# Kernel tuning notes

Measured on AMD Instinct MI355X. Metric: run time of the kernel, lower is better.

Reference implementation:

```python
import jax, jax.numpy as jnp
import numpy as np

D_MODEL = 1024
NUM_HEADS = 16
D_K = D_MODEL // NUM_HEADS


def setup_inputs() -> dict:
    key = jax.random.key(0)
    ks = jax.random.split(key, 11)
    B, S = 2, 2048
    scale = 1.0 / np.sqrt(D_MODEL)
    inp = {
        'Q': jax.random.normal(ks[0], (B, S, D_MODEL), dtype=jnp.float32),
        'K': jax.random.normal(ks[1], (B, S, D_MODEL), dtype=jnp.float32),
        'V': jax.random.normal(ks[2], (B, S, D_MODEL), dtype=jnp.float32),
        'Wq': jax.random.normal(ks[3], (D_MODEL, D_MODEL), dtype=jnp.float32) * scale,
        'bq': jax.random.normal(ks[4], (D_MODEL,), dtype=jnp.float32) * scale,
        'Wk': jax.random.normal(ks[5], (D_MODEL, D_MODEL), dtype=jnp.float32) * scale,
        'bk': jax.random.normal(ks[6], (D_MODEL,), dtype=jnp.float32) * scale,
        'Wv': jax.random.normal(ks[7], (D_MODEL, D_MODEL), dtype=jnp.float32) * scale,
        'bv': jax.random.normal(ks[8], (D_MODEL,), dtype=jnp.float32) * scale,
        'Wo': jax.random.normal(ks[9], (D_MODEL, D_MODEL), dtype=jnp.float32) * scale,
        'bo': jax.random.normal(ks[10], (D_MODEL,), dtype=jnp.float32) * scale,
    }
    return inp


def _split_heads(x):
    B, S, _ = x.shape
    return x.reshape(B, S, NUM_HEADS, D_K).transpose(0, 2, 1, 3)  # [B,H,S,dk]


def reference(Q, K, V, Wq, bq, Wk, bk, Wv, bv, Wo, bo):
    # Linear projections (torch Linear: x @ W.T + b)
    q = _split_heads(Q @ Wq.T + bq)
    k = _split_heads(K @ Wk.T + bk)
    v = _split_heads(V @ Wv.T + bv)
    scores = jnp.einsum('bhqd,bhkd->bhqk', q, k) / jnp.sqrt(jnp.float32(D_K))
    probs = jax.nn.softmax(scores, axis=-1)
    out = jnp.einsum('bhqk,bhkd->bhqd', probs, v)  # [B,H,S,dk]
    B, H, S, dk = out.shape
    out = out.transpose(0, 2, 1, 3).reshape(B, S, D_MODEL)
    return out @ Wo.T + bo
```

## Files before the change

### kernel.cpp

```cpp
#include <hip/hip_runtime.h>
#include <hip/hip_bf16.h>

#define DEV __device__ __forceinline__

#define BATCH 2
#define SEQ   2048
#define DMODEL 1024
#define NHEAD 16
#define DK    64
#define MROWS (BATCH*SEQ)
#define KD    1024
#define GEMM_NT (KD/32)

#define QSCALE 0.18033688011112042f

typedef __attribute__((ext_vector_type(4))) float f32x4;
typedef __attribute__((ext_vector_type(8))) short s16x8;
typedef __attribute__((ext_vector_type(4))) float fvec4;
typedef __attribute__((ext_vector_type(2))) unsigned int u32x2;
typedef __attribute__((ext_vector_type(4))) unsigned int u32x4;

__device__ short g_X[3][MROWS*DMODEL];
__device__ short g_W[4][DMODEL*DMODEL];
__device__ short g_q [MROWS*DMODEL];
__device__ short g_k [MROWS*DMODEL];
__device__ short g_vt[MROWS*DMODEL];
__device__ short g_at[MROWS*DMODEL];

DEV short f2bf(float f) {
  union { __hip_bfloat16 h; short s; } u;
  u.h = __float2bfloat16(f);
  return u.s;
}

DEV unsigned int f2bf2(float lo, float hi) {
  unsigned int r;
  asm("v_cvt_pk_bf16_f32 %0, %1, %2" : "=v"(r) : "v"(lo), "v"(hi));
  return r;
}

DEV float fexp2(float x) {
  float r;
  asm("v_exp_f32 %0, %1" : "=v"(r) : "v"(x));
  return r;
}

DEV void gload_lds16(const void* g, void* l) {
  __builtin_amdgcn_global_load_lds(
      (const __attribute__((address_space(1))) void*)g,
      (__attribute__((address_space(3))) void*)l, 16, 0, 0);
}

DEV f32x4 mfma16(s16x8 a, s16x8 b, f32x4 c) {
  return __builtin_amdgcn_mfma_f32_16x16x32_bf16(a, b, c, 0, 0, 0);
}

__global__ __launch_bounds__(256)
void cast_all(const float* __restrict__ q, const float* __restrict__ k,
              const float* __restrict__ v, const float* __restrict__ wq,
              const float* __restrict__ wk, const float* __restrict__ wv,
              const float* __restrict__ wo) {
  int z = blockIdx.z;
  const float* src;
  short* dst;
  int n8;
  if (z < 3) {
    src = z == 0 ? q : z == 1 ? k : v;
    dst = g_X[z];
    n8 = MROWS*DMODEL/8;
  } else {
    src = z == 3 ? wq : z == 4 ? wk : z == 5 ? wv : wo;
    dst = g_W[z - 3];
    n8 = DMODEL*DMODEL/8;
  }
  int i = blockIdx.x * 256 + threadIdx.x;
  if (i < n8) {
    const fvec4* p = (const fvec4*)(src + (size_t)i*8);
    fvec4 v0 = p[0], v1 = p[1];
    u32x4 r;
    r[0] = f2bf2(v0[0], v0[1]); r[1] = f2bf2(v0[2], v0[3]);
    r[2] = f2bf2(v1[0], v1[1]); r[3] = f2bf2(v1[2], v1[3]);
    *(u32x4*)(dst + (size_t)i*8) = r;
  }
}

struct GemmSmem { short As[2][128*32]; short Bs[2][128*32]; };

DEV void gemm_core(GemmSmem& sm, const short* __restrict__ A,
                   const short* __restrict__ Bw, const float* __restrict__ bias,
                   void* __restrict__ outp, float scale, int mode,
                   int rowBase, int colBase) {
  const int t = threadIdx.x, l = t & 63, w = t >> 6, g = l >> 4;
  const int wr = w >> 1, wc = w & 1;

  f32x4 acc[4][4] = {};

  auto stage = [&](int buf, int k0) {
#pragma unroll
    for (int j = 0; j < 2; ++j) {
      int e = w*1024 + j*512 + l*8;
      int e2 = e ^ (((e >> 7) & 3) << 3);
      int r = e2 >> 5, c = e2 & 31;
      gload_lds16(A  + (size_t)(rowBase + r)*KD + k0 + c, &sm.As[buf][w*1024 + j*512]);
      gload_lds16(Bw + (size_t)(colBase + r)*KD + k0 + c, &sm.Bs[buf][w*1024 + j*512]);
    }
  };

  stage(0, 0);
  stage(1, 32);

  for (int i = 0; i < GEMM_NT; ++i) {
    if (i < GEMM_NT - 1) asm volatile("s_waitcnt vmcnt(4)" ::: "memory");
    else                 asm volatile("s_waitcnt vmcnt(0)" ::: "memory");
    __builtin_amdgcn_s_barrier();
    __builtin_amdgcn_sched_barrier(0);

    const int cur = i & 1;
    s16x8 a[4], b[4];
#pragma unroll
    for (int x = 0; x < 4; ++x) {
      int ra = wr*64 + x*16 + (l & 15);
      int ia = (ra*32 + g*8) ^ (((ra >> 2) & 3) << 3);
      a[x] = *(const s16x8*)&sm.As[cur][ia];
      int rb = wc*64 + x*16 + (l & 15);
      int ib = (rb*32 + g*8) ^ (((rb >> 2) & 3) << 3);
      b[x] = *(const s16x8*)&sm.Bs[cur][ib];
    }

    __builtin_amdgcn_s_setprio(1);
#pragma unroll
    for (int x = 0; x < 4; ++x)
#pragma unroll
      for (int jn = 0; jn < 4; ++jn)
        acc[x][jn] = mfma16(a[x], b[jn], acc[x][jn]);
    __builtin_amdgcn_s_setprio(0);

    __builtin_amdgcn_s_barrier();
    __builtin_amdgcn_sched_barrier(0);
    if (i + 2 < GEMM_NT) stage(cur, (i + 2)*32);
  }

#pragma unroll
  for (int x = 0; x < 4; ++x) {
    int mrow0 = rowBase + wr*64 + x*16 + g*4;
#pragma unroll
    for (int jn = 0; jn < 4; ++jn) {
      int n = colBase + wc*64 + jn*16 + (l & 15);
      float bv = bias[n];
      float val[4];
#pragma unroll
      for (int r = 0; r < 4; ++r) val[r] = (acc[x][jn][r] + bv) * scale;
      if (mode == 3) {
#pragma unroll
        for (int r = 0; r < 4; ++r)
          ((float*)outp)[(size_t)(mrow0 + r)*DMODEL + n] = val[r];
      } else {
        unsigned int pk0 = f2bf2(val[0], val[1]);
        unsigned int pk1 = f2bf2(val[2], val[3]);
        int h = n >> 6, d = n & 63;
#pragma unroll
        for (int r = 0; r < 4; ++r) {
          int m = mrow0 + r;
          int b = m >> 11, s = m & 2047;
          unsigned int pk = r < 2 ? pk0 : pk1;
          short sv = (short)((r & 1) ? (pk >> 16) : (pk & 0xffff));
          if (mode == 1)
            ((short*)outp)[(((size_t)(b*NHEAD + h)*SEQ + s)*DK) + d] = sv;
          else
            ((short*)outp)[((size_t)(b*NHEAD + h)*DK + d)*SEQ + s] = sv;
        }
      }
    }
  }
}

__global__ __launch_bounds__(256, 4)
void proj_qkv(const float* __restrict__ bq, const float* __restrict__ bk,
              const float* __restrict__ bv) {
  __shared__ GemmSmem sm;
  int z = blockIdx.z;
  int orig = blockIdx.y*8 + blockIdx.x;
  int swz = (orig & 7)*32 + (orig >> 3);
  int bx = swz & 7, by = swz >> 3;
  const float* bias = z == 0 ? bq : z == 1 ? bk : bv;
  void* outp = z == 0 ? (void*)g_q : z == 1 ? (void*)g_k : (void*)g_vt;
  gemm_core(sm, g_X[z], g_W[z], bias, outp, z == 0 ? QSCALE : 1.0f,
            z == 2 ? 2 : 1, by*128, bx*128);
}

__global__ __launch_bounds__(256, 4)
void proj_out(const float* __restrict__ bo, float* __restrict__ out) {
  __shared__ GemmSmem sm;
  int orig = blockIdx.y*8 + blockIdx.x;
  int swz = (orig & 7)*32 + (orig >> 3);
  int bx = swz & 7, by = swz >> 3;
  gemm_core(sm, g_at, g_W[3], bo, out, 1.0f, 3, by*128, bx*128);
}

__global__ __launch_bounds__(512, 4)
void attn_kernel(short* __restrict__ aout) {
  __shared__ short ks[4][64*64];
  __shared__ short vs[4][64*64];

  const int t = threadIdx.x, l = t & 63, w = t >> 6, g = l >> 4;
  const int q15 = l & 15;
  const int qg = w & 3, kp = w >> 2;
  int orig = blockIdx.y*16 + blockIdx.x;
  int swz = (orig & 7)*64 + (orig >> 3);
  const int qblk = swz & 15, bh = swz >> 4;
  const int qbase = qblk * 128;
  const size_t hoff = (size_t)bh * SEQ * DK;

  auto stage_pair = [&](int pr) {
    int e = t*8;
    int e2 = e ^ (((e >> 6) & 7) << 3);
    int t0 = 2*pr, t1 = t0 + 1;
    gload_lds16(g_k + hoff + (size_t)(t0*64)*DK + e2, &ks[t0 & 3][e]);
    gload_lds16(g_k + hoff + (size_t)(t1*64)*DK + e2, &ks[t1 & 3][e]);
    gload_lds16(g_vt + hoff + (size_t)(e2 >> 6)*SEQ + t0*64 + (e2 & 63), &vs[t0 & 3][e]);
    gload_lds16(g_vt + hoff + (size_t)(e2 >> 6)*SEQ + t1*64 + (e2 & 63), &vs[t1 & 3][e]);
  };

  s16x8 qf[2][2];
  {
    const short* q0 = g_q + hoff + (size_t)(qbase + qg*32 + q15)*DK;
    qf[0][0] = *(const s16x8*)(q0 + g*8);
    qf[0][1] = *(const s16x8*)(q0 + 32 + g*8);
    qf[1][0] = *(const s16x8*)(q0 + 16*DK + g*8);
    qf[1][1] = *(const s16x8*)(q0 + 16*DK + 32 + g*8);
  }
  stage_pair(0);

  float lsum[2] = {0.f, 0.f};
  f32x4 o[2][4] = {};

  for (int i = 0; i < 16; ++i) {
    asm volatile("s_waitcnt vmcnt(0)" ::: "memory");
    __builtin_amdgcn_s_barrier();
    __builtin_amdgcn_sched_barrier(0);
    if (i + 1 < 16) stage_pair(i + 1);

    const short* kb = ks[(2*i + kp) & 3];
    const short* vb = vs[(2*i + kp) & 3];

    f32x4 sc[2][4] = {};
    __builtin_amdgcn_s_setprio(1);
#pragma unroll
    for (int ni = 0; ni < 4; ++ni) {
      int row = ni*16 + q15;
      int sx = (row & 7) << 3;
      s16x8 k0 = *(const s16x8*)&kb[(row*64 + g*8) ^ sx];
      s16x8 k1 = *(const s16x8*)&kb[(row*64 + 32 + g*8) ^ sx];
      sc[0][ni] = mfma16(k0, qf[0][0], sc[0][ni]);
      sc[0][ni] = mfma16(k1, qf[0][1], sc[0][ni]);
      sc[1][ni] = mfma16(k0, qf[1][0], sc[1][ni]);
      sc[1][ni] = mfma16(k1, qf[1][1], sc[1][ni]);
    }
    __builtin_amdgcn_s_setprio(0);

    s16x8 pa[2][2];
#pragma unroll
    for (int grp = 0; grp < 2; ++grp) {
      float p[4][4];
#pragma unroll
      for (int ni = 0; ni < 4; ++ni)
#pragma unroll
        for (int r = 0; r < 4; ++r)
          p[ni][r] = fexp2(sc[grp][ni][r]);
      float s0 = (p[0][0]+p[0][1]) + (p[0][2]+p[0][3]);
      float s1 = (p[1][0]+p[1][1]) + (p[1][2]+p[1][3]);
      float s2 = (p[2][0]+p[2][1]) + (p[2][2]+p[2][3]);
      float s3 = (p[3][0]+p[3][1]) + (p[3][2]+p[3][3]);
      lsum[grp] += (s0+s1) + (s2+s3);

      unsigned pk[4][2];
#pragma unroll
      for (int ni = 0; ni < 4; ++ni) {
        pk[ni][0] = f2bf2(p[ni][0], p[ni][1]);
        pk[ni][1] = f2bf2(p[ni][2], p[ni][3]);
      }
#pragma unroll
      for (int kf = 0; kf < 2; ++kf) {
        u32x4 P4;
#pragma unroll
        for (int u = 0; u < 2; ++u) {
          unsigned x = pk[2*kf][u], y = pk[2*kf + 1][u];
          asm("v_permlane32_swap_b32 %0, %1" : "+v"(x), "+v"(y));
          asm("v_permlane16_swap_b32 %0, %1" : "+v"(x), "+v"(y));
          P4[u]     = x;
          P4[2 + u] = y;
        }
        union { u32x4 u4; s16x8 s8; } cv;
        cv.u4 = P4;
        pa[grp][kf] = cv.s8;
      }
    }

    __builtin_amdgcn_s_setprio(1);
#pragma unroll
    for (int nd = 0; nd < 4; ++nd) {
      int row = nd*16 + q15;
      int sx = (row & 7) << 3;
      s16x8 v0 = *(const s16x8*)&vb[(row*64 + g*8) ^ sx];
      s16x8 v1 = *(const s16x8*)&vb[(row*64 + 32 + g*8) ^ sx];
      o[0][nd] = mfma16(pa[0][0], v0, o[0][nd]);
      o[0][nd] = mfma16(pa[0][1], v1, o[0][nd]);
      o[1][nd] = mfma16(pa[1][0], v0, o[1][nd]);
      o[1][nd] = mfma16(pa[1][1], v1, o[1][nd]);
    }
    __builtin_amdgcn_s_setprio(0);
  }

  __syncthreads();
  float* ob = (float*)&vs[0][0];
  float* lb = (float*)&ks[0][0];
  if (kp) {
#pragma unroll
    for (int grp = 0; grp < 2; ++grp) {
#pragma unroll
      for (int nd = 0; nd < 4; ++nd)
#pragma unroll
        for (int r = 0; r < 4; ++r)
          ob[(qg*32 + grp*16 + nd*4 + r)*64 + l] = o[grp][nd][r];
      lb[(qg*2 + grp)*64 + l] = lsum[grp];
    }
  }
  __syncthreads();
  if (!kp) {
    int b = bh >> 4, h = bh & 15;
#pragma unroll
    for (int grp = 0; grp < 2; ++grp) {
#pragma unroll
      for (int nd = 0; nd < 4; ++nd)
#pragma unroll
        for (int r = 0; r < 4; ++r)
          o[grp][nd][r] += ob[(qg*32 + grp*16 + nd*4 + r)*64 + l];
      float ls = lsum[grp] + lb[(qg*2 + grp)*64 + l];
      ls += __shfl_xor(ls, 16);
      ls += __shfl_xor(ls, 32);
      float inv = 1.0f / ls;
      float iv[4];
#pragma unroll
      for (int r = 0; r < 4; ++r)
        iv[r] = __shfl(inv, (l & 48) | (g*4 + r));
#pragma unroll
      for (int nd = 0; nd < 4; ++nd) {
        int dcol = h*DK + nd*16 + q15;
#pragma unroll
        for (int r = 0; r < 4; ++r) {
          int srow = qbase + qg*32 + grp*16 + g*4 + r;
          aout[((size_t)(b*SEQ + srow))*DMODEL + dcol] = f2bf(o[grp][nd][r] * iv[r]);
        }
      }
    }
  }
}

extern "C" void kernel_launch(void* const* d_in, const int* in_sizes, int n_in,
                              void* d_out, int out_size, void* d_ws, size_t ws_size,
                              hipStream_t stream) {
  const float* Q  = (const float*)d_in[0];
  const float* K  = (const float*)d_in[1];
  const float* V  = (const float*)d_in[2];
  const float* Wq = (const float*)d_in[3];
  const float* bq = (const float*)d_in[4];
  const float* Wk = (const float*)d_in[5];
  const float* bk = (const float*)d_in[6];
  const float* Wv = (const float*)d_in[7];
  const float* bv = (const float*)d_in[8];
  const float* Wo = (const float*)d_in[9];
  const float* bo = (const float*)d_in[10];

  short* pat;
  hipGetSymbolAddress((void**)&pat, HIP_SYMBOL(g_at));

  const int nX8 = MROWS*DMODEL/8;
  dim3 blk(256);

  cast_all<<<dim3(nX8/256, 1, 7), blk, 0, stream>>>(Q, K, V, Wq, Wk, Wv, Wo);
  proj_qkv<<<dim3(DMODEL/128, MROWS/128, 3), blk, 0, stream>>>(bq, bk, bv);
  attn_kernel<<<dim3(SEQ/128, BATCH*NHEAD), dim3(512), 0, stream>>>(pat);
  proj_out<<<dim3(DMODEL/128, MROWS/128), blk, 0, stream>>>(bo, (float*)d_out);
}
```

Baseline: 136.4 us.

## Use 256x256 tiles with triple-buffered LDS pipeline for QKV projection GEMM

Replaces the shared 128x128 GEMM core for the QKV projections with a dedicated 512-thread kernel that computes 256x256 output tiles, using a 3-stage LDS buffer and split half-tile loads interleaved with MFMA phases. The larger tile raises arithmetic intensity and cuts global reloads, and the deeper pipeline aims to hide load latency. The grid shrinks to 192 blocks, which may underfill the 256 CUs and raises register and LDS pressure. The output projection is specialised inline with its epilogue simplified to fp32 stores.

```diff
diff --git a/kernel.cpp b/kernel.cpp
--- a/kernel.cpp
+++ b/kernel.cpp
@@ -84,14 +84,138 @@
   }
 }
 
+struct Gemm8Smem { short As[3][256*32]; short Bs[3][256*32]; };
+
+__global__ __launch_bounds__(512, 2)
+void proj_qkv(const float* __restrict__ bq, const float* __restrict__ bk,
+              const float* __restrict__ bv) {
+  __shared__ Gemm8Smem sm;
+  const int t = threadIdx.x, l = t & 63, g = l >> 4, q15 = l & 15;
+  const int w = t >> 6, wm = w >> 2, wn = w & 3;
+  const int z = blockIdx.z;
+  const short* A  = g_X[z];
+  const short* Bw = g_W[z];
+  const float* bias = z == 0 ? bq : z == 1 ? bk : bv;
+  void* outp = z == 0 ? (void*)g_q : z == 1 ? (void*)g_k : (void*)g_vt;
+  const float scale = z == 0 ? QSCALE : 1.0f;
+  const int mode = z == 2 ? 2 : 1;
+  const int rowBase = blockIdx.y * 256;
+  const int colBase = blockIdx.x * 256;
+
+  f32x4 acc[8][4] = {};
+
+  auto stageA = [&](int buf, int tt, int m) {
+    int e = m*4096 + t*8;
+    int e2 = e ^ (((e >> 7) & 3) << 3);
+    gload_lds16(A + (size_t)(rowBase + (e2 >> 5))*KD + tt*32 + (e2 & 31),
+                &sm.As[buf][e]);
+  };
+  auto stageB = [&](int buf, int tt, int m) {
+    int e = m*4096 + t*8;
+    int e2 = e ^ (((e >> 7) & 3) << 3);
+    gload_lds16(Bw + (size_t)(colBase + (e2 >> 5))*KD + tt*32 + (e2 & 31),
+                &sm.Bs[buf][e]);
+  };
+
+  stageA(0, 0, 0); stageB(0, 0, 0); stageA(0, 0, 1); stageB(0, 0, 1);
+  stageA(1, 1, 0); stageB(1, 1, 0); stageA(1, 1, 1); stageB(1, 1, 1);
+  asm volatile("s_waitcnt vmcnt(4)" ::: "memory");
+  __builtin_amdgcn_s_barrier();
+  __builtin_amdgcn_sched_barrier(0);
+
+  int cur = 0, nxt = 2;
+  for (int i = 0; i < GEMM_NT; ++i) {
+    const int tt2 = (i + 2) & (GEMM_NT - 1);
+
+    s16x8 a[8], b[2];
+#pragma unroll
+    for (int mf = 0; mf < 8; ++mf) {
+      int row = wm*128 + mf*16 + q15;
+      a[mf] = *(const s16x8*)&sm.As[cur][(row*32 + g*8) ^ (((row >> 2) & 3) << 3)];
+    }
+#pragma unroll
+    for (int nf = 0; nf < 2; ++nf) {
+      int row = wn*64 + nf*16 + q15;
+      b[nf] = *(const s16x8*)&sm.Bs[cur][(row*32 + g*8) ^ (((row >> 2) & 3) << 3)];
+    }
+    stageA(nxt, tt2, 0); stageB(nxt, tt2, 0);
+    __builtin_amdgcn_s_barrier();
+    __builtin_amdgcn_sched_barrier(0);
+    __builtin_amdgcn_s_setprio(1);
+#pragma unroll
+    for (int mf = 0; mf < 8; ++mf)
+#pragma unroll
+      for (int nf = 0; nf < 2; ++nf)
+        acc[mf][nf] = mfma16(a[mf], b[nf], acc[mf][nf]);
+    __builtin_amdgcn_s_setprio(0);
+    __builtin_amdgcn_s_barrier();
+    __builtin_amdgcn_sched_barrier(0);
+
+#pragma unroll
+    for (int nf = 0; nf < 2; ++nf) {
+      int row = wn*64 + (nf + 2)*16 + q15;
+      b[nf] = *(const s16x8*)&sm.Bs[cur][(row*32 + g*8) ^ (((row >> 2) & 3) << 3)];
+    }
+    stageA(nxt, tt2, 1); stageB(nxt, tt2, 1);
+    __builtin_amdgcn_s_barrier();
+    __builtin_amdgcn_sched_barrier(0);
+    __builtin_amdgcn_s_setprio(1);
+#pragma unroll
+    for (int mf = 0; mf < 8; ++mf)
+#pragma unroll
+      for (int nf = 0; nf < 2; ++nf)
+        acc[mf][nf + 2] = mfma16(a[mf], b[nf], acc[mf][nf + 2]);
+    __builtin_amdgcn_s_setprio(0);
+    asm volatile("s_waitcnt vmcnt(4)" ::: "memory");
+    __builtin_amdgcn_s_barrier();
+    __builtin_amdgcn_sched_barrier(0);
+
+    cur = cur == 2 ? 0 : cur + 1;
+    nxt = nxt == 2 ? 0 : nxt + 1;
+  }
+  asm volatile("s_waitcnt vmcnt(0)" ::: "memory");
+
+#pragma unroll
+  for (int mf = 0; mf < 8; ++mf) {
+    int mrow0 = rowBase + wm*128 + mf*16 + g*4;
+#pragma unroll
+    for (int nf = 0; nf < 4; ++nf) {
+      int n = colBase + wn*64 + nf*16 + q15;
+      float bv = bias[n];
+      float val[4];
+#pragma unroll
+      for (int r = 0; r < 4; ++r) val[r] = (acc[mf][nf][r] + bv) * scale;
+      unsigned int pk0 = f2bf2(val[0], val[1]);
+      unsigned int pk1 = f2bf2(val[2], val[3]);
+      int h = n >> 6, d = n & 63;
+#pragma unroll
+      for (int r = 0; r < 4; ++r) {
+        int m = mrow0 + r;
+        int b = m >> 11, s = m & 2047;
+        unsigned int pk = r < 2 ? pk0 : pk1;
+        short sv = (short)((r & 1) ? (pk >> 16) : (pk & 0xffff));
+        if (mode == 1)
+          ((short*)outp)[(((size_t)(b*NHEAD + h)*SEQ + s)*DK) + d] = sv;
+        else
+          ((short*)outp)[((size_t)(b*NHEAD + h)*DK + d)*SEQ + s] = sv;
+      }
+    }
+  }
+}
+
 struct GemmSmem { short As[2][128*32]; short Bs[2][128*32]; };
 
-DEV void gemm_core(GemmSmem& sm, const short* __restrict__ A,
-                   const short* __restrict__ Bw, const float* __restrict__ bias,
-                   void* __restrict__ outp, float scale, int mode,
-                   int rowBase, int colBase) {
+__global__ __launch_bounds__(256, 4)
+void proj_out(const float* __restrict__ bo, float* __restrict__ out) {
+  __shared__ GemmSmem sm;
   const int t = threadIdx.x, l = t & 63, w = t >> 6, g = l >> 4;
   const int wr = w >> 1, wc = w & 1;
+  int orig = blockIdx.y*8 + blockIdx.x;
+  int swz = (orig & 7)*32 + (orig >> 3);
+  int bx = swz & 7, by = swz >> 3;
+  const int rowBase = by*128, colBase = bx*128;
+  const short* A = g_at;
+  const short* Bw = g_W[3];
 
   f32x4 acc[4][4] = {};
 
@@ -146,55 +270,12 @@
 #pragma unroll
     for (int jn = 0; jn < 4; ++jn) {
       int n = colBase + wc*64 + jn*16 + (l & 15);
-      float bv = bias[n];
-      float val[4];
-#pragma unroll
-      for (int r = 0; r < 4; ++r) val[r] = (acc[x][jn][r] + bv) * scale;
-      if (mode == 3) {
-#pragma unroll
-        for (int r = 0; r < 4; ++r)
-          ((float*)outp)[(size_t)(mrow0 + r)*DMODEL + n] = val[r];
-      } else {
-        unsigned int pk0 = f2bf2(val[0], val[1]);
-        unsigned int pk1 = f2bf2(val[2], val[3]);
-        int h = n >> 6, d = n & 63;
-#pragma unroll
-        for (int r = 0; r < 4; ++r) {
-          int m = mrow0 + r;
-          int b = m >> 11, s = m & 2047;
-          unsigned int pk = r < 2 ? pk0 : pk1;
-          short sv = (short)((r & 1) ? (pk >> 16) : (pk & 0xffff));
-          if (mode == 1)
-            ((short*)outp)[(((size_t)(b*NHEAD + h)*SEQ + s)*DK) + d] = sv;
-          else
-            ((short*)outp)[((size_t)(b*NHEAD + h)*DK + d)*SEQ + s] = sv;
-        }
-      }
-    }
-  }
-}
-
-__global__ __launch_bounds__(256, 4)
-void proj_qkv(const float* __restrict__ bq, const float* __restrict__ bk,
-              const float* __restrict__ bv) {
-  __shared__ GemmSmem sm;
-  int z = blockIdx.z;
-  int orig = blockIdx.y*8 + blockIdx.x;
-  int swz = (orig & 7)*32 + (orig >> 3);
-  int bx = swz & 7, by = swz >> 3;
-  const float* bias = z == 0 ? bq : z == 1 ? bk : bv;
-  void* outp = z == 0 ? (void*)g_q : z == 1 ? (void*)g_k : (void*)g_vt;
-  gemm_core(sm, g_X[z], g_W[z], bias, outp, z == 0 ? QSCALE : 1.0f,
-            z == 2 ? 2 : 1, by*128, bx*128);
-}
-
-__global__ __launch_bounds__(256, 4)
-void proj_out(const float* __restrict__ bo, float* __restrict__ out) {
-  __shared__ GemmSmem sm;
-  int orig = blockIdx.y*8 + blockIdx.x;
-  int swz = (orig & 7)*32 + (orig >> 3);
-  int bx = swz & 7, by = swz >> 3;
-  gemm_core(sm, g_at, g_W[3], bo, out, 1.0f, 3, by*128, bx*128);
+      float bv = bo[n];
+#pragma unroll
+      for (int r = 0; r < 4; ++r)
+        out[(size_t)(mrow0 + r)*DMODEL + n] = acc[x][jn][r] + bv;
+    }
+  }
 }
 
 __global__ __launch_bounds__(512, 4)
@@ -378,7 +459,7 @@
   dim3 blk(256);
 
   cast_all<<<dim3(nX8/256, 1, 7), blk, 0, stream>>>(Q, K, V, Wq, Wk, Wv, Wo);
-  proj_qkv<<<dim3(DMODEL/128, MROWS/128, 3), blk, 0, stream>>>(bq, bk, bv);
+  proj_qkv<<<dim3(4, 16, 3), dim3(512), 0, stream>>>(bq, bk, bv);
   attn_kernel<<<dim3(SEQ/128, BATCH*NHEAD), dim3(512), 0, stream>>>(pat);
-  proj_out<<<dim3(DMODEL/128, MROWS/128), blk, 0, stream>>>(bo, (float*)d_out);
-}
+  proj_out<<<dim3(8, 32), blk, 0, stream>>>(bo, (float*)d_out);
+}
```

Measured after the change: 147.4 us. 1.08x slower.

## Triple-buffer GEMM LDS staging and split QKV projection into separate launches

Applied to the files above, without the earlier changes.

The projection GEMM moves from double to triple LDS buffering. The prefetch of tile i+2 is now issued right after the current tile's fragments are read, which removes the second barrier per K-step. The single 3D-grid QKV projection launch becomes three separate 256-block launches of one unified proj_gemm kernel, with pointers taken from symbol addresses on the host. In exchange, shared memory per block grows and launch bounds drop to 3 blocks per CU, and the three serial launches lose the concurrency of the 768-block grid.

```diff
diff --git a/kernel.cpp b/kernel.cpp
--- a/kernel.cpp
+++ b/kernel.cpp
@@ -84,14 +84,18 @@
   }
 }
 
-struct GemmSmem { short As[2][128*32]; short Bs[2][128*32]; };
-
-DEV void gemm_core(GemmSmem& sm, const short* __restrict__ A,
-                   const short* __restrict__ Bw, const float* __restrict__ bias,
-                   void* __restrict__ outp, float scale, int mode,
-                   int rowBase, int colBase) {
+struct GemmSmem { short As[3][128*32]; short Bs[3][128*32]; };
+
+__global__ __launch_bounds__(256, 3)
+void proj_gemm(const short* __restrict__ A, const short* __restrict__ Bw,
+               const float* __restrict__ bias, void* __restrict__ outp,
+               float scale, int mode) {
+  __shared__ GemmSmem sm;
   const int t = threadIdx.x, l = t & 63, w = t >> 6, g = l >> 4;
   const int wr = w >> 1, wc = w & 1;
+  int orig = blockIdx.y*8 + blockIdx.x;
+  int swz = (orig & 7)*32 + (orig >> 3);
+  const int rowBase = (swz >> 3)*128, colBase = (swz & 7)*128;
 
   f32x4 acc[4][4] = {};
 
@@ -109,13 +113,13 @@
   stage(0, 0);
   stage(1, 32);
 
+  int cur = 0, nxt = 2;
   for (int i = 0; i < GEMM_NT; ++i) {
     if (i < GEMM_NT - 1) asm volatile("s_waitcnt vmcnt(4)" ::: "memory");
     else                 asm volatile("s_waitcnt vmcnt(0)" ::: "memory");
     __builtin_amdgcn_s_barrier();
     __builtin_amdgcn_sched_barrier(0);
 
-    const int cur = i & 1;
     s16x8 a[4], b[4];
 #pragma unroll
     for (int x = 0; x < 4; ++x) {
@@ -126,6 +130,8 @@
       int ib = (rb*32 + g*8) ^ (((rb >> 2) & 3) << 3);
       b[x] = *(const s16x8*)&sm.Bs[cur][ib];
     }
+    if (i + 2 < GEMM_NT) stage(nxt, (i + 2)*32);
+    __builtin_amdgcn_sched_barrier(0);
 
     __builtin_amdgcn_s_setprio(1);
 #pragma unroll
@@ -135,9 +141,8 @@
         acc[x][jn] = mfma16(a[x], b[jn], acc[x][jn]);
     __builtin_amdgcn_s_setprio(0);
 
-    __builtin_amdgcn_s_barrier();
-    __builtin_amdgcn_sched_barrier(0);
-    if (i + 2 < GEMM_NT) stage(cur, (i + 2)*32);
+    cur = cur == 2 ? 0 : cur + 1;
+    nxt = nxt == 2 ? 0 : nxt + 1;
   }
 
 #pragma unroll
@@ -172,29 +177,6 @@
       }
     }
   }
-}
-
-__global__ __launch_bounds__(256, 4)
-void proj_qkv(const float* __restrict__ bq, const float* __restrict__ bk,
-              const float* __restrict__ bv) {
-  __shared__ GemmSmem sm;
-  int z = blockIdx.z;
-  int orig = blockIdx.y*8 + blockIdx.x;
-  int swz = (orig & 7)*32 + (orig >> 3);
-  int bx = swz & 7, by = swz >> 3;
-  const float* bias = z == 0 ? bq : z == 1 ? bk : bv;
-  void* outp = z == 0 ? (void*)g_q : z == 1 ? (void*)g_k : (void*)g_vt;
-  gemm_core(sm, g_X[z], g_W[z], bias, outp, z == 0 ? QSCALE : 1.0f,
-            z == 2 ? 2 : 1, by*128, bx*128);
-}
-
-__global__ __launch_bounds__(256, 4)
-void proj_out(const float* __restrict__ bo, float* __restrict__ out) {
-  __shared__ GemmSmem sm;
-  int orig = blockIdx.y*8 + blockIdx.x;
-  int swz = (orig & 7)*32 + (orig >> 3);
-  int bx = swz & 7, by = swz >> 3;
-  gemm_core(sm, g_at, g_W[3], bo, out, 1.0f, 3, by*128, bx*128);
 }
 
 __global__ __launch_bounds__(512, 4)
@@ -371,14 +353,24 @@
   const float* Wo = (const float*)d_in[9];
   const float* bo = (const float*)d_in[10];
 
-  short* pat;
+  short *pX, *pW, *pq, *pk, *pvt, *pat;
+  hipGetSymbolAddress((void**)&pX,  HIP_SYMBOL(g_X));
+  hipGetSymbolAddress((void**)&pW,  HIP_SYMBOL(g_W));
+  hipGetSymbolAddress((void**)&pq,  HIP_SYMBOL(g_q));
+  hipGetSymbolAddress((void**)&pk,  HIP_SYMBOL(g_k));
+  hipGetSymbolAddress((void**)&pvt, HIP_SYMBOL(g_vt));
   hipGetSymbolAddress((void**)&pat, HIP_SYMBOL(g_at));
 
   const int nX8 = MROWS*DMODEL/8;
+  const size_t NX = (size_t)MROWS*DMODEL;
+  const size_t NW = (size_t)DMODEL*DMODEL;
   dim3 blk(256);
+  dim3 gP(8, 32);
 
   cast_all<<<dim3(nX8/256, 1, 7), blk, 0, stream>>>(Q, K, V, Wq, Wk, Wv, Wo);
-  proj_qkv<<<dim3(DMODEL/128, MROWS/128, 3), blk, 0, stream>>>(bq, bk, bv);
+  proj_gemm<<<gP, blk, 0, stream>>>(pX,        pW,        bq, pq,  QSCALE, 1);
+  proj_gemm<<<gP, blk, 0, stream>>>(pX + NX,   pW + NW,   bk, pk,  1.0f,   1);
+  proj_gemm<<<gP, blk, 0, stream>>>(pX + 2*NX, pW + 2*NW, bv, pvt, 1.0f,   2);
   attn_kernel<<<dim3(SEQ/128, BATCH*NHEAD), dim3(512), 0, stream>>>(pat);
-  proj_out<<<dim3(DMODEL/128, MROWS/128), blk, 0, stream>>>(bo, (float*)d_out);
-}
+  proj_gemm<<<gP, blk, 0, stream>>>(pat, pW + 3*NW, bo, (float*)d_out, 1.0f, 3);
+}
```

Result: slower. 143.2 us (+5.0%).

## Triple-buffer GEMM LDS pipeline and stage V-transpose epilogue through LDS

Applied to the files above, without the earlier changes.

Moves the GEMM mainloop from double to triple buffering in LDS. The next-next tile is now issued right after the fragment reads, which removes the second barrier per k-step. The transposed V projection epilogue now writes bf16 results into LDS with an XOR swizzle and then stores 16-byte contiguous rows along the sequence, replacing scattered 2-byte global stores. The larger LDS footprint lowers launch bounds occupancy from 4 to 3 blocks per CU.

```diff
diff --git a/kernel.cpp b/kernel.cpp
--- a/kernel.cpp
+++ b/kernel.cpp
@@ -84,13 +84,14 @@
   }
 }
 
-struct GemmSmem { short As[2][128*32]; short Bs[2][128*32]; };
+struct GemmSmem { short As[3][128*32]; short Bs[3][128*32]; };
 
 DEV void gemm_core(GemmSmem& sm, const short* __restrict__ A,
                    const short* __restrict__ Bw, const float* __restrict__ bias,
                    void* __restrict__ outp, float scale, int mode,
                    int rowBase, int colBase) {
   const int t = threadIdx.x, l = t & 63, w = t >> 6, g = l >> 4;
+  const int q15 = l & 15;
   const int wr = w >> 1, wc = w & 1;
 
   f32x4 acc[4][4] = {};
@@ -109,23 +110,25 @@
   stage(0, 0);
   stage(1, 32);
 
+  int cur = 0, nxt = 2;
   for (int i = 0; i < GEMM_NT; ++i) {
     if (i < GEMM_NT - 1) asm volatile("s_waitcnt vmcnt(4)" ::: "memory");
     else                 asm volatile("s_waitcnt vmcnt(0)" ::: "memory");
     __builtin_amdgcn_s_barrier();
     __builtin_amdgcn_sched_barrier(0);
 
-    const int cur = i & 1;
     s16x8 a[4], b[4];
 #pragma unroll
     for (int x = 0; x < 4; ++x) {
-      int ra = wr*64 + x*16 + (l & 15);
+      int ra = wr*64 + x*16 + q15;
       int ia = (ra*32 + g*8) ^ (((ra >> 2) & 3) << 3);
       a[x] = *(const s16x8*)&sm.As[cur][ia];
-      int rb = wc*64 + x*16 + (l & 15);
+      int rb = wc*64 + x*16 + q15;
       int ib = (rb*32 + g*8) ^ (((rb >> 2) & 3) << 3);
       b[x] = *(const s16x8*)&sm.Bs[cur][ib];
     }
+    if (i + 2 < GEMM_NT) stage(nxt, (i + 2)*32);
+    __builtin_amdgcn_sched_barrier(0);
 
     __builtin_amdgcn_s_setprio(1);
 #pragma unroll
@@ -135,9 +138,40 @@
         acc[x][jn] = mfma16(a[x], b[jn], acc[x][jn]);
     __builtin_amdgcn_s_setprio(0);
 
-    __builtin_amdgcn_s_barrier();
-    __builtin_amdgcn_sched_barrier(0);
-    if (i + 2 < GEMM_NT) stage(cur, (i + 2)*32);
+    cur = cur == 2 ? 0 : cur + 1;
+    nxt = nxt == 2 ? 0 : nxt + 1;
+  }
+
+  if (mode == 2) {
+    short* ct = (short*)&sm;
+    __syncthreads();
+#pragma unroll
+    for (int x = 0; x < 4; ++x) {
+      int m0 = wr*64 + x*16 + g*4;
+#pragma unroll
+      for (int jn = 0; jn < 4; ++jn) {
+        int n = wc*64 + jn*16 + q15;
+        float bv = bias[colBase + n];
+        u32x2 w2;
+        w2[0] = f2bf2(acc[x][jn][0] + bv, acc[x][jn][1] + bv);
+        w2[1] = f2bf2(acc[x][jn][2] + bv, acc[x][jn][3] + bv);
+        int mi = m0 ^ ((n & 15) << 3);
+        *(u32x2*)&ct[n*128 + mi] = w2;
+      }
+    }
+    __syncthreads();
+    int c = t & 1, n = t >> 1;
+    int ng = colBase + n;
+    int h = ng >> 6, d = ng & 63;
+    int b = rowBase >> 11;
+    int s0 = (rowBase & 2047) + c*64;
+    short* dst = (short*)outp + ((size_t)(b*NHEAD + h)*DK + d)*SEQ + s0;
+#pragma unroll
+    for (int j = 0; j < 8; ++j) {
+      int mi = (c*64 + j*8) ^ ((n & 15) << 3);
+      *(s16x8*)&dst[j*8] = *(const s16x8*)&ct[n*128 + mi];
+    }
+    return;
   }
 
 #pragma unroll
@@ -145,7 +179,7 @@
     int mrow0 = rowBase + wr*64 + x*16 + g*4;
 #pragma unroll
     for (int jn = 0; jn < 4; ++jn) {
-      int n = colBase + wc*64 + jn*16 + (l & 15);
+      int n = colBase + wc*64 + jn*16 + q15;
       float bv = bias[n];
       float val[4];
 #pragma unroll
@@ -164,17 +198,14 @@
           int b = m >> 11, s = m & 2047;
           unsigned int pk = r < 2 ? pk0 : pk1;
           short sv = (short)((r & 1) ? (pk >> 16) : (pk & 0xffff));
-          if (mode == 1)
-            ((short*)outp)[(((size_t)(b*NHEAD + h)*SEQ + s)*DK) + d] = sv;
-          else
-            ((short*)outp)[((size_t)(b*NHEAD + h)*DK + d)*SEQ + s] = sv;
+          ((short*)outp)[(((size_t)(b*NHEAD + h)*SEQ + s)*DK) + d] = sv;
         }
       }
     }
   }
 }
 
-__global__ __launch_bounds__(256, 4)
+__global__ __launch_bounds__(256, 3)
 void proj_qkv(const float* __restrict__ bq, const float* __restrict__ bk,
               const float* __restrict__ bv) {
   __shared__ GemmSmem sm;
@@ -188,7 +219,7 @@
             z == 2 ? 2 : 1, by*128, bx*128);
 }
 
-__global__ __launch_bounds__(256, 4)
+__global__ __launch_bounds__(256, 3)
 void proj_out(const float* __restrict__ bo, float* __restrict__ out) {
   __shared__ GemmSmem sm;
   int orig = blockIdx.y*8 + blockIdx.x;
@@ -378,7 +409,7 @@
   dim3 blk(256);
 
   cast_all<<<dim3(nX8/256, 1, 7), blk, 0, stream>>>(Q, K, V, Wq, Wk, Wv, Wo);
-  proj_qkv<<<dim3(DMODEL/128, MROWS/128, 3), blk, 0, stream>>>(bq, bk, bv);
+  proj_qkv<<<dim3(8, 32, 3), blk, 0, stream>>>(bq, bk, bv);
   attn_kernel<<<dim3(SEQ/128, BATCH*NHEAD), dim3(512), 0, stream>>>(pat);
-  proj_out<<<dim3(DMODEL/128, MROWS/128), blk, 0, stream>>>(bo, (float*)d_out);
-}
+  proj_out<<<dim3(8, 32), blk, 0, stream>>>(bo, (float*)d_out);
+}
```

New measurement: 128.5 us (median of 2 runs). 1.06x faster.
